# Kernel optimization log

Hardware: AMD Instinct MI355X
Metric: run time of the kernel (lower is better)

The kernel has to match this reference:

```python
import jax, jax.numpy as jnp
import numpy as np

B, K, BIN = 16, 2048, 256
GRU, EMB, HID = 1024, 1024, 1024
H, KV = 16, 4
D = HID // H          # 64 head dim
NREP = H // KV        # 4 GQA repeat factor


def rotate_half(x):
    x1, x2 = jnp.split(x, 2, axis=-1)
    return jnp.concatenate((-x2, x1), axis=-1)


def setup_inputs() -> dict:
    key = jax.random.key(0)
    ks = jax.random.split(key, 8)
    h = jax.random.normal(ks[0], (B, K, GRU), dtype=jnp.float32)
    # real RoPE frequency tables, shape (BIN, D)
    inv_freq = 1.0 / (10000.0 ** (jnp.arange(0, D, 2, dtype=jnp.float32) / D))
    t = jnp.arange(BIN, dtype=jnp.float32)
    freqs = jnp.outer(t, inv_freq)                      # (BIN, D/2)
    emb = jnp.concatenate((freqs, freqs), axis=-1)      # (BIN, D)
    freqs_cos, freqs_sin = jnp.cos(emb), jnp.sin(emb)
    s = lambda fan: 1.0 / np.sqrt(fan).astype(np.float32)
    Wq = jax.random.normal(ks[1], (H * D, EMB), jnp.float32) * s(EMB)
    Wk = jax.random.normal(ks[2], (KV * D, GRU), jnp.float32) * s(GRU)
    Wv = jax.random.normal(ks[3], (KV * D, GRU), jnp.float32) * s(GRU)
    Wo = jax.random.normal(ks[4], (EMB, H * D), jnp.float32) * s(H * D)
    output_queries = jax.random.normal(ks[5], (BIN, EMB), jnp.float32)
    Wr = jax.random.normal(ks[6], (2, EMB), jnp.float32) * s(EMB)
    br = jnp.zeros((2,), jnp.float32)
    return {"h": h, "freqs_cos": freqs_cos, "freqs_sin": freqs_sin,
            "Wq": Wq, "Wk": Wk, "Wv": Wv, "Wo": Wo,
            "output_queries": output_queries, "Wr": Wr, "br": br}


def reference(h, freqs_cos, freqs_sin, Wq, Wk, Wv, Wo, output_queries, Wr, br):
    # KV projections from GRU history: (B, K, KV, D)
    k = (h @ Wk.T).reshape(B, K, KV, D)
    v = (h @ Wv.T).reshape(B, K, KV, D)
    # Queries are batch-invariant learned tokens: (BIN, H, D)
    q = (output_queries @ Wq.T).reshape(BIN, H, D)
    cos = freqs_cos[:, None, :]  # (BIN, 1, D) broadcast over heads
    sin = freqs_sin[:, None, :]
    q = q * cos + rotate_half(q) * sin
    # GQA: repeat_interleave KV heads to H heads
    k_rep = jnp.repeat(k, NREP, axis=2)  # (B, K, H, D)
    v_rep = jnp.repeat(v, NREP, axis=2)
    scores = jnp.einsum('qhd,bkhd->bhqk', q, k_rep) / np.sqrt(D).astype(np.float32)
    attn = jax.nn.softmax(scores, axis=-1)               # dropout p=0 (eval)
    out = jnp.einsum('bhqk,bkhd->bqhd', attn, v_rep).reshape(B, BIN, H * D)
    z = out @ Wo.T                                        # (B, BIN, EMB)
    return z @ Wr.T + br                                  # (B, BIN, 2)
```

## Files before the change

### kernel.cpp

```cpp
#include <hip/hip_runtime.h>

typedef __attribute__((ext_vector_type(8))) short short8;
typedef __attribute__((ext_vector_type(4))) float f32x4;
typedef __attribute__((ext_vector_type(16))) float f32x16;

#define DEV static __device__ __forceinline__

DEV unsigned short f2bf(float f) {
  unsigned int u = __float_as_uint(f);
  u += 0x7fff + ((u >> 16) & 1);
  return (unsigned short)(u >> 16);
}

DEV unsigned int cvtpk(float lo, float hi) {
  unsigned int r;
  asm("v_cvt_pk_bf16_f32 %0, %1, %2" : "=v"(r) : "v"(lo), "v"(hi));
  return r;
}

DEV float max3f(float a, float b, float c) {
  float r;
  asm("v_max3_f32 %0, %1, %2, %3" : "=v"(r) : "v"(a), "v"(b), "v"(c));
  return r;
}

DEV f32x4 mfma16(short8 a, short8 b, f32x4 c) {
  return __builtin_amdgcn_mfma_f32_16x16x32_bf16(a, b, c, 0, 0, 0);
}

DEV f32x16 mfma32(short8 a, short8 b, f32x16 c) {
  return __builtin_amdgcn_mfma_f32_32x32x16_bf16(a, b, c, 0, 0, 0);
}

DEV void gl_lds16(const void* g, void* l) {
  __builtin_amdgcn_global_load_lds((const __attribute__((address_space(1))) void*)g,
                                   (__attribute__((address_space(3))) void*)l, 16, 0, 0);
}

__global__ __launch_bounds__(256) void cvtB_kernel(const float* __restrict__ Wq,
                                                   const float* __restrict__ Wk,
                                                   const float* __restrict__ Wv,
                                                   unsigned short* __restrict__ wqb,
                                                   unsigned short* __restrict__ wkvb) {
  int id = blockIdx.x * 256 + threadIdx.x;
  int e = id * 4;
  float4 v;
  unsigned short* d;
  if (e < 1048576)      { v = *(const float4*)(Wq + e);             d = wqb + e; }
  else if (e < 1310720) { v = *(const float4*)(Wk + (e - 1048576)); d = wkvb + (e - 1048576); }
  else                  { v = *(const float4*)(Wv + (e - 1310720)); d = wkvb + 262144 + (e - 1310720); }
  uint2 pk;
  pk.x = cvtpk(v.x, v.y);
  pk.y = cvtpk(v.z, v.w);
  *(uint2*)d = pk;
}

__global__ __launch_bounds__(256) void wrp_partial(const float* __restrict__ Wr,
                                                   const float* __restrict__ Wo,
                                                   float* __restrict__ part) {
  int blk = blockIdx.x;
  int tid = threadIdx.x;
  float a0[4] = {0.f,0.f,0.f,0.f};
  float a1[4] = {0.f,0.f,0.f,0.f};
  int e0 = blk * 64;
  for (int e = e0; e < e0 + 64; e++) {
    float w0 = Wr[e];
    float w1 = Wr[1024 + e];
    #pragma unroll
    for (int j4 = 0; j4 < 4; j4++) {
      float wo = Wo[(size_t)e * 1024 + j4 * 256 + tid];
      a0[j4] += w0 * wo;
      a1[j4] += w1 * wo;
    }
  }
  #pragma unroll
  for (int j4 = 0; j4 < 4; j4++) {
    part[blk * 2048 + 0    + j4 * 256 + tid] = a0[j4];
    part[blk * 2048 + 1024 + j4 * 256 + tid] = a1[j4];
  }
}

__global__ __launch_bounds__(256) void wrp_reduce(const float* __restrict__ part,
                                                  float* __restrict__ Wrp) {
  int id = blockIdx.x * 256 + threadIdx.x;
  float s = 0.f;
  #pragma unroll
  for (int blk = 0; blk < 16; blk++) s += part[blk * 2048 + id];
  Wrp[id] = s;
}

__global__ __launch_bounds__(512, 2) void gemm_kv(const float* __restrict__ A,
                                                  const unsigned short* __restrict__ Bb,
                                                  unsigned short* __restrict__ ok,
                                                  unsigned short* __restrict__ vrm) {
  __shared__ unsigned short Asl[3][4096];
  __shared__ unsigned short Bsl[3][16384];

  int bid = blockIdx.x;
  int sw = (bid & 7) * 32 + (bid >> 3);
  int m0 = sw * 128;

  int tid = threadIdx.x;
  int w = tid >> 6, l = tid & 63;
  int l4 = l >> 4, l15 = l & 15;

  int arow = tid >> 2, ac = tid & 3;
  const float* ga = A + (size_t)(m0 + arow) * 1024 + ac * 8;
  int awb = arow * 64 + ((ac ^ ((arow >> 1) & 3)) * 16);

  const unsigned short* gbB = Bb + (size_t)(tid >> 2) * 1024
                                 + (((tid & 3) ^ ((tid >> 3) & 3)) * 8);

  int fsw = (l4 ^ ((l15 >> 1) & 3)) * 16;
  int aoff = l15 * 64 + fsw;
  int boff = (w * 64 + l15) * 64 + fsw;

  f32x4 acc[8][4];
  #pragma unroll
  for (int i = 0; i < 8; i++)
    #pragma unroll
    for (int j = 0; j < 4; j++) acc[i][j] = (f32x4)(0.f);

  float4 aXx, aXy, aYx, aYy;

  #define LOADA(T, RX, RY)                                                  \
    { const float* gA = ga + (T) * 32;                                      \
      RX = *(const float4*)(gA);                                            \
      RY = *(const float4*)(gA + 4); }

  #define STAGEB(SB, T)                                                     \
    { const unsigned short* b0p = gbB + (T) * 32;                           \
      gl_lds16(b0p,          (char*)Bsl[SB] + tid * 16);                    \
      gl_lds16(b0p + 131072, (char*)Bsl[SB] + 8192  + tid * 16);            \
      gl_lds16(b0p + 262144, (char*)Bsl[SB] + 16384 + tid * 16);            \
      gl_lds16(b0p + 393216, (char*)Bsl[SB] + 24576 + tid * 16); }

  #define WRITEA(WB, RX, RY)                                                \
    { union { short8 s; unsigned int u[4]; } af;                            \
      af.u[0] = cvtpk(RX.x, RX.y); af.u[1] = cvtpk(RX.z, RX.w);             \
      af.u[2] = cvtpk(RY.x, RY.y); af.u[3] = cvtpk(RY.z, RY.w);             \
      *(short8*)((char*)Asl[WB] + awb) = af.s; }

  #define COMPUTE(CB)                                                       \
    { const char* Ab = (const char*)Asl[CB];                                \
      const char* Bf = (const char*)Bsl[CB];                                \
      short8 bfr[4];                                                        \
      _Pragma("unroll")                                                     \
      for (int j = 0; j < 4; j++)                                           \
        bfr[j] = *(const short8*)(Bf + boff + j * 1024);                    \
      __builtin_amdgcn_s_setprio(1);                                        \
      _Pragma("unroll")                                                     \
      for (int i = 0; i < 8; i++) {                                         \
        short8 af = *(const short8*)(Ab + aoff + i * 1024);                 \
        _Pragma("unroll")                                                   \
        for (int j = 0; j < 4; j++)                                         \
          acc[i][j] = mfma16(af, bfr[j], acc[i][j]);                        \
      }                                                                     \
      __builtin_amdgcn_s_setprio(0); }

  #define ENDSTEP                                                           \
    { asm volatile("s_waitcnt vmcnt(6)" ::: "memory");                      \
      asm volatile("s_waitcnt lgkmcnt(0)" ::: "memory");                    \
      __builtin_amdgcn_s_barrier();                                         \
      __builtin_amdgcn_sched_barrier(0); }

  LOADA(0, aXx, aXy);
  STAGEB(0, 0);
  WRITEA(0, aXx, aXy);
  LOADA(1, aXx, aXy);
  STAGEB(1, 1);
  asm volatile("s_waitcnt vmcnt(6)" ::: "memory");
  asm volatile("s_waitcnt lgkmcnt(0)" ::: "memory");
  __builtin_amdgcn_s_barrier();
  __builtin_amdgcn_sched_barrier(0);

  #define STEPE(T, CB, WB, SB)                                              \
    { LOADA((T) + 2, aYx, aYy); STAGEB(SB, (T) + 2);                        \
      COMPUTE(CB); WRITEA(WB, aXx, aXy); ENDSTEP }
  #define STEPO(T, CB, WB, SB)                                              \
    { LOADA((T) + 2, aXx, aXy); STAGEB(SB, (T) + 2);                        \
      COMPUTE(CB); WRITEA(WB, aYx, aYy); ENDSTEP }

  #pragma unroll 1
  for (int tb = 0; tb < 30; tb += 6) {
    STEPE(tb + 0, 0, 1, 2);
    STEPO(tb + 1, 1, 2, 0);
    STEPE(tb + 2, 2, 0, 1);
    STEPO(tb + 3, 0, 1, 2);
    STEPE(tb + 4, 1, 2, 0);
    STEPO(tb + 5, 2, 0, 1);
  }
  COMPUTE(0);
  WRITEA(1, aXx, aXy);
  asm volatile("s_waitcnt vmcnt(0)" ::: "memory");
  asm volatile("s_waitcnt lgkmcnt(0)" ::: "memory");
  __builtin_amdgcn_s_barrier();
  __builtin_amdgcn_sched_barrier(0);
  COMPUTE(1);

  #undef LOADA
  #undef STAGEB
  #undef WRITEA
  #undef COMPUTE
  #undef ENDSTEP
  #undef STEPE
  #undef STEPO

  #pragma unroll
  for (int i = 0; i < 8; i++)
    #pragma unroll
    for (int j = 0; j < 4; j++) {
      int n = w * 64 + j * 16 + l15;
      int kvv = n >> 6, d = n & 63;
      #pragma unroll
      for (int r = 0; r < 4; r++) {
        int m = m0 + i * 16 + l4 * 4 + r;
        int bb = m >> 11, kk = m & 2047;
        unsigned short val = f2bf(acc[i][j][r]);
        if (kvv < 4)
          ok[((size_t)(bb * 4 + kvv) * 2048 + kk) * 64 + d] = val;
        else
          vrm[((size_t)(bb * 4 + (kvv - 4)) * 2048 + kk) * 64 + d] = val;
      }
    }
}

__global__ __launch_bounds__(256) void vtr_kernel(const unsigned short* __restrict__ vrm,
                                                  unsigned short* __restrict__ vt) {
  __shared__ unsigned short T[64][72];
  int g = blockIdx.x >> 5;
  int kt = blockIdx.x & 31;
  int tid = threadIdx.x;
  int r = tid >> 2, c0 = (tid & 3) * 16;

  const unsigned short* src = vrm + ((size_t)g * 2048 + kt * 64) * 64;
  *(short8*)&T[r][c0]     = *(const short8*)(src + (size_t)r * 64 + c0);
  *(short8*)&T[r][c0 + 8] = *(const short8*)(src + (size_t)r * 64 + c0 + 8);
  __syncthreads();

  int d = tid >> 2;
  unsigned short* dst = vt + (size_t)g * 131072 + (size_t)d * 2048 + kt * 64 + (tid & 3) * 16;
  short8 o0, o1;
  #pragma unroll
  for (int j = 0; j < 8; j++) {
    o0[j] = (short)T[(tid & 3) * 16 + j][d];
    o1[j] = (short)T[(tid & 3) * 16 + 8 + j][d];
  }
  *(short8*)dst = o0;
  *(short8*)(dst + 8) = o1;
}

__global__ __launch_bounds__(256) void gemm_q(const float* __restrict__ A,
                                              const unsigned short* __restrict__ Bb,
                                              float* __restrict__ of) {
  __shared__ unsigned short Asm[2][4096];
  __shared__ unsigned short Bsm[2][4096];

  int bid = blockIdx.x;
  int ksplit = bid >> 4;
  int m0 = ((bid >> 3) & 1) * 128;
  int n0 = (bid & 7) * 128;
  int t0 = ksplit * 8;
  constexpr int nt = 8;

  int tid = threadIdx.x;
  int w = tid >> 6, l = tid & 63;
  int l4 = l >> 4, l15 = l & 15;
  int wm = w >> 1, wn = w & 1;

  int ra = w * 32 + (l >> 1);
  int rx = (l >> 2) & 3;
  const float* ga = A + (size_t)(m0 + ra) * 1024 + t0 * 32 + (l & 1) * 16;
  int pw0 = (2 * (l & 1) + 0) ^ rx;
  int pw1 = (2 * (l & 1) + 1) ^ rx;
  int awb0 = ra * 64 + pw0 * 16;
  int awb1 = ra * 64 + pw1 * 16;

  int rb = w * 32 + (l >> 2);
  int cb = ((l & 3) ^ ((l >> 3) & 3)) * 8;
  const unsigned short* gb = Bb + (size_t)(n0 + rb) * 1024 + t0 * 32 + cb;

  int qsw = l4 ^ ((l15 >> 1) & 3);
  int arb = (wm * 64 + l15) * 64 + qsw * 16;
  int brb = (wn * 64 + l15) * 64 + qsw * 16;

  f32x4 acc[4][4];
  #pragma unroll
  for (int i = 0; i < 4; i++)
    #pragma unroll
    for (int j = 0; j < 4; j++) acc[i][j] = (f32x4)(0.f);

  float4 fa0, fa1, fa2, fa3;

  #define LOADA(tt)                                                        \
    { const float* gA = ga + (tt) * 32;                                    \
      fa0 = *(const float4*)(gA);                                          \
      fa1 = *(const float4*)(gA + 4);                                      \
      fa2 = *(const float4*)(gA + 8);                                      \
      fa3 = *(const float4*)(gA + 12); }

  #define WRITEA(bufi)                                                     \
    { union { short8 s; unsigned int u[4]; } t0u, t1u;                     \
      t0u.u[0] = cvtpk(fa0.x, fa0.y); t0u.u[1] = cvtpk(fa0.z, fa0.w);      \
      t0u.u[2] = cvtpk(fa1.x, fa1.y); t0u.u[3] = cvtpk(fa1.z, fa1.w);      \
      t1u.u[0] = cvtpk(fa2.x, fa2.y); t1u.u[1] = cvtpk(fa2.z, fa2.w);      \
      t1u.u[2] = cvtpk(fa3.x, fa3.y); t1u.u[3] = cvtpk(fa3.z, fa3.w);      \
      *(short8*)((char*)Asm[bufi] + awb0) = t0u.s;                         \
      *(short8*)((char*)Asm[bufi] + awb1) = t1u.s; }

  #define STAGEB(bufi, tt)                                                 \
    { char* lb = (char*)Bsm[bufi] + w * 2048;                              \
      const unsigned short* gB = gb + (tt) * 32;                           \
      gl_lds16(gB, lb);                                                    \
      gl_lds16(gB + 16384, lb + 1024); }

  LOADA(0);
  STAGEB(0, 0);
  WRITEA(0);
  __syncthreads();

  for (int t = 0; t < nt; t++) {
    int buf = t & 1;
    if (t + 1 < nt) {
      LOADA(t + 1);
      STAGEB(buf ^ 1, t + 1);
    }
    short8 af[4], bfg[4];
    #pragma unroll
    for (int i = 0; i < 4; i++)
      af[i] = *(const short8*)((char*)Asm[buf] + arb + i * 1024);
    #pragma unroll
    for (int j = 0; j < 4; j++)
      bfg[j] = *(const short8*)((char*)Bsm[buf] + brb + j * 1024);
    #pragma unroll
    for (int i = 0; i < 4; i++)
      #pragma unroll
      for (int j = 0; j < 4; j++)
        acc[i][j] = mfma16(af[i], bfg[j], acc[i][j]);
    if (t + 1 < nt) WRITEA(buf ^ 1);
    __syncthreads();
  }
  #undef LOADA
  #undef WRITEA
  #undef STAGEB

  float* o = of + (size_t)ksplit * 262144;
  #pragma unroll
  for (int i = 0; i < 4; i++)
    #pragma unroll
    for (int j = 0; j < 4; j++) {
      int n = n0 + wn * 64 + j * 16 + l15;
      #pragma unroll
      for (int r = 0; r < 4; r++) {
        int m = m0 + wm * 64 + i * 16 + l4 * 4 + r;
        o[(size_t)m * 1024 + n] = acc[i][j][r];
      }
    }
}

__global__ __launch_bounds__(256) void rope_kernel(const float* __restrict__ qp,
                                                   const float* __restrict__ cosb,
                                                   const float* __restrict__ sinb,
                                                   unsigned short* __restrict__ qb) {
  int id = blockIdx.x * 256 + threadIdx.x;
  int qrow = id >> 10, hd = id & 1023, hh = hd >> 6, d = hd & 63;
  int od = hh * 64 + ((d < 32) ? d + 32 : d - 32);
  float v = 0.f, o = 0.f;
  #pragma unroll
  for (int s4 = 0; s4 < 4; s4++) {
    v += qp[s4 * 262144 + qrow * 1024 + hd];
    o += qp[s4 * 262144 + qrow * 1024 + od];
  }
  if (d < 32) o = -o;
  float c = cosb[qrow * 64 + d];
  float s = sinb[qrow * 64 + d];
  float outv = (v * c + o * s) * 0.18033688011112042f;
  qb[((size_t)hh * 256 + qrow) * 64 + d] = f2bf(outv);
}

__global__ __launch_bounds__(256) void attn_kernel(const unsigned short* __restrict__ qb,
                                                   const unsigned short* __restrict__ kb,
                                                   const unsigned short* __restrict__ vb,
                                                   const float* __restrict__ Wrp,
                                                   float* __restrict__ part) {
  __shared__ unsigned short Kt[3][4096];
  __shared__ unsigned short Vt[3][4096];

  int bid = blockIdx.x;
  int x = bid & 7, mid = (bid >> 3) & 7, top2 = bid >> 6;
  int g = mid * 8 + x;
  int b = g >> 2, kvh = g & 3;
  int split = top2 >> 3;
  int top = top2 & 7;
  int hl = top >> 1, qh = top & 1;
  int h = kvh * 4 + hl;

  int tid = threadIdx.x;
  int w = tid >> 6, l = tid & 63;
  int q31 = l & 31, L = l >> 5;
  int qg = qh * 128 + w * 32 + q31;

  const unsigned short* kg = kb + (size_t)(b * 4 + kvh) * 2048 * 64;
  const unsigned short* vg = vb + (size_t)(b * 4 + kvh) * 64 * 2048;

  short8 qf[4];
  #pragma unroll
  for (int c = 0; c < 4; c++)
    qf[c] = *(const short8*)&qb[((size_t)h * 256 + qg) * 64 + c * 16 + L * 8];

  f32x16 Ot[2];
  Ot[0] = (f32x16)(0.f); Ot[1] = (f32x16)(0.f);
  float m = -1e30f, lsum = 0.f;

  int ksrow = tid >> 3, kslot = tid & 7;
  const unsigned short* ksrc = kg + (size_t)ksrow * 64 + ((kslot ^ (ksrow & 7)) * 8);
  int vsrow = tid >> 2, vslot = tid & 3;
  const unsigned short* vsrc = vg + (size_t)vsrow * 2048 + ((vslot ^ ((vsrow >> 1) & 3)) * 8);

  int tb0 = split * 16;

  #define STAGE(bufi, tt)                                                       \
    { gl_lds16(ksrc + (size_t)((tt) * 2 + 0) * 2048, (char*)Kt[bufi] + tid * 16);        \
      gl_lds16(ksrc + (size_t)((tt) * 2 + 1) * 2048, (char*)Kt[bufi] + 4096 + tid * 16); \
      gl_lds16(vsrc + ((tt) * 2 + 0) * 32,           (char*)Vt[bufi] + tid * 16);        \
      gl_lds16(vsrc + ((tt) * 2 + 1) * 32,           (char*)Vt[bufi] + 4096 + tid * 16); }

  #define COMPUTE(CB)                                                           \
    _Pragma("unroll")                                                           \
    for (int sub = 0; sub < 2; sub++) {                                         \
      const char* Kb = (const char*)Kt[CB] + sub * 4096;                        \
      const char* Vb = (const char*)Vt[CB] + sub * 4096;                        \
      f32x16 st = (f32x16)(0.f);                                                \
      _Pragma("unroll")                                                         \
      for (int c = 0; c < 4; c++) {                                             \
        int row = q31;                                                          \
        int byt = row * 128 + (((c * 2 + L) ^ (row & 7)) * 16);                 \
        short8 kf = *(const short8*)(Kb + byt);                                 \
        st = mfma32(kf, qf[c], st);                                             \
      }                                                                         \
      float g0 = max3f(st[0], st[1], st[2]);                                    \
      float g1 = max3f(st[3], st[4], st[5]);                                    \
      float g2 = max3f(st[6], st[7], st[8]);                                    \
      float g3 = max3f(st[9], st[10], st[11]);                                  \
      float g4 = max3f(st[12], st[13], st[14]);                                 \
      float mx = fmaxf(max3f(g0, g1, g2), max3f(g3, g4, st[15]));               \
      mx = fmaxf(mx, __shfl_xor(mx, 32));                                       \
      if (!__all(mx <= m + 8.f)) {                                              \
        float mnew = fmaxf(m, mx);                                              \
        float corr = exp2f(m - mnew);                                           \
        lsum *= corr;                                                           \
        _Pragma("unroll")                                                       \
        for (int db = 0; db < 2; db++)                                          \
          _Pragma("unroll")                                                     \
          for (int r = 0; r < 16; r++) Ot[db][r] *= corr;                       \
        m = mnew;                                                               \
      }                                                                         \
      float p[16];                                                              \
      float ls = 0.f;                                                           \
      _Pragma("unroll")                                                         \
      for (int r = 0; r < 16; r++) {                                            \
        p[r] = exp2f(st[r] - m);                                                \
        ls += p[r];                                                             \
      }                                                                         \
      lsum += ls;                                                               \
      unsigned int pw[2][4];                                                    \
      _Pragma("unroll")                                                         \
      for (int kc = 0; kc < 2; kc++) {                                          \
        unsigned int A0 = cvtpk(p[kc * 8 + 0], p[kc * 8 + 1]);                  \
        unsigned int A1 = cvtpk(p[kc * 8 + 2], p[kc * 8 + 3]);                  \
        unsigned int B0 = cvtpk(p[kc * 8 + 4], p[kc * 8 + 5]);                  \
        unsigned int B1 = cvtpk(p[kc * 8 + 6], p[kc * 8 + 7]);                  \
        asm volatile("v_permlane32_swap_b32 %0, %1" : "+v"(A0), "+v"(B0));      \
        asm volatile("v_permlane32_swap_b32 %0, %1" : "+v"(A1), "+v"(B1));      \
        pw[kc][0] = A0; pw[kc][1] = A1; pw[kc][2] = B0; pw[kc][3] = B1;         \
      }                                                                         \
      _Pragma("unroll")                                                         \
      for (int db = 0; db < 2; db++) {                                          \
        int drow = db * 32 + q31;                                               \
        _Pragma("unroll")                                                       \
        for (int kc = 0; kc < 2; kc++) {                                        \
          int byt = drow * 64 + (((kc * 2 + L) ^ ((drow >> 1) & 3)) * 16);      \
          short8 vf = *(const short8*)(Vb + byt);                               \
          short8 pf;                                                            \
          {                                                                     \
            union { short8 s; unsigned int u[4]; } uu;                          \
            uu.u[0] = pw[kc][0]; uu.u[1] = pw[kc][1];                           \
            uu.u[2] = pw[kc][2]; uu.u[3] = pw[kc][3];                           \
            pf = uu.s;                                                          \
          }                                                                     \
          Ot[db] = mfma32(vf, pf, Ot[db]);                                      \
        }                                                                       \
      }                                                                         \
    }

  #define E8                                                                    \
    { asm volatile("s_waitcnt vmcnt(8)" ::: "memory");                          \
      __builtin_amdgcn_s_barrier();                                             \
      __builtin_amdgcn_sched_barrier(0); }

  STAGE(0, tb0 + 0);
  STAGE(1, tb0 + 1);
  asm volatile("s_waitcnt vmcnt(8)" ::: "memory");
  __builtin_amdgcn_s_barrier();
  __builtin_amdgcn_sched_barrier(0);

  #pragma unroll 1
  for (int tb = 0; tb < 12; tb += 3) {
    STAGE(2, tb0 + tb + 2); COMPUTE(0) E8;
    STAGE(0, tb0 + tb + 3); COMPUTE(1) E8;
    STAGE(1, tb0 + tb + 4); COMPUTE(2) E8;
  }
  STAGE(2, tb0 + 14); COMPUTE(0) E8;
  STAGE(0, tb0 + 15); COMPUTE(1) E8;
  COMPUTE(2)
  asm volatile("s_waitcnt vmcnt(0)" ::: "memory");
  __builtin_amdgcn_s_barrier();
  __builtin_amdgcn_sched_barrier(0);
  COMPUTE(0)

  #undef STAGE
  #undef COMPUTE
  #undef E8

  lsum += __shfl_xor(lsum, 32);

  float a0 = 0.f, a1 = 0.f;
  #pragma unroll
  for (int db = 0; db < 2; db++)
    #pragma unroll
    for (int rq = 0; rq < 4; rq++) {
      int dbase = db * 32 + rq * 8 + L * 4;
      float4 w0v = *(const float4*)(Wrp + h * 64 + dbase);
      float4 w1v = *(const float4*)(Wrp + 1024 + h * 64 + dbase);
      #pragma unroll
      for (int j = 0; j < 4; j++) {
        float o = Ot[db][rq * 4 + j];
        a0 += o * ((const float*)&w0v)[j];
        a1 += o * ((const float*)&w1v)[j];
      }
    }
  a0 += __shfl_xor(a0, 32);
  a1 += __shfl_xor(a1, 32);

  if (L == 0) {
    size_t base = ((((size_t)(b * 16 + h) * 256 + qg) * 2) + split) * 4;
    float4 r4;
    r4.x = m; r4.y = lsum; r4.z = a0; r4.w = a1;
    *(float4*)&part[base] = r4;
  }
}

__global__ __launch_bounds__(256) void final_kernel(const float* __restrict__ part,
                                                    const float* __restrict__ br,
                                                    float* __restrict__ out) {
  int id = blockIdx.x * 256 + threadIdx.x;
  int c = id & 1, q = (id >> 1) & 255, b = id >> 9;
  float s = br[c];
  #pragma unroll
  for (int hh = 0; hh < 16; hh++) {
    size_t base = (((size_t)(b * 16 + hh) * 256 + q) * 2) * 4;
    float4 f0 = *(const float4*)&part[base];
    float4 f1 = *(const float4*)&part[base + 4];
    float mm = fmaxf(f0.x, f1.x);
    float w0 = exp2f(f0.x - mm), w1 = exp2f(f1.x - mm);
    float den = w0 * f0.y + w1 * f1.y;
    float num = (c == 0) ? (w0 * f0.z + w1 * f1.z) : (w0 * f0.w + w1 * f1.w);
    s += num / den;
  }
  out[id] = s;
}

extern "C" void kernel_launch(void* const* d_in, const int* in_sizes, int n_in,
                              void* d_out, int out_size, void* d_ws, size_t ws_size,
                              hipStream_t stream) {
  const float* h    = (const float*)d_in[0];
  const float* fcos = (const float*)d_in[1];
  const float* fsin = (const float*)d_in[2];
  const float* Wq   = (const float*)d_in[3];
  const float* Wk   = (const float*)d_in[4];
  const float* Wv   = (const float*)d_in[5];
  const float* Wo   = (const float*)d_in[6];
  const float* oq   = (const float*)d_in[7];
  const float* Wr   = (const float*)d_in[8];
  const float* br   = (const float*)d_in[9];
  float* out = (float*)d_out;

  char* ws = (char*)d_ws;
  unsigned short* kbuf = (unsigned short*)(ws);
  unsigned short* vbuf = (unsigned short*)(ws + 16777216);
  float* qpart         = (float*)(ws + 33554432);
  unsigned short* qbf  = (unsigned short*)(ws + 37748736);
  float* wpart         = (float*)(ws + 38273024);
  float* Wrp           = (float*)(ws + 38404096);
  float* apart         = (float*)(ws + 38412288);
  unsigned short* wqb  = (unsigned short*)(ws + 42606592);
  unsigned short* wkvb = (unsigned short*)(ws + 44703744);
  unsigned short* vrm  = (unsigned short*)(ws + 45752320);

  cvtB_kernel<<<dim3(1536), dim3(256), 0, stream>>>(Wq, Wk, Wv, wqb, wkvb);
  wrp_partial<<<dim3(16), dim3(256), 0, stream>>>(Wr, Wo, wpart);
  wrp_reduce<<<dim3(8), dim3(256), 0, stream>>>(wpart, Wrp);
  gemm_q<<<dim3(64), dim3(256), 0, stream>>>(oq, wqb, qpart);
  rope_kernel<<<dim3(1024), dim3(256), 0, stream>>>(qpart, fcos, fsin, qbf);
  gemm_kv<<<dim3(256), dim3(512), 0, stream>>>(h, wkvb, kbuf, vrm);
  vtr_kernel<<<dim3(2048), dim3(256), 0, stream>>>(vrm, vbuf);
  attn_kernel<<<dim3(1024), dim3(256), 0, stream>>>(qbf, kbuf, vbuf, Wrp, apart);
  final_kernel<<<dim3(32), dim3(256), 0, stream>>>(apart, br, out);
}
```

Measured before the change: 147.6 us.

## Replace triple-buffered gemm_kv pipeline with a simpler double-buffered loop

The KV projection GEMM moves from a three-stage LDS ring with two-deep prefetch and vmcnt(6) partial waits to a two-buffer ping-pong loop that prefetches one tile ahead and waits for all loads (vmcnt(0)) each step. This cuts LDS per block by a third and drops one set of A staging registers, which could raise occupancy. In exchange it reduces how far global loads can run ahead of compute, so memory latency is more exposed, and the loop is no longer hand-unrolled.

```diff
diff --git a/kernel.cpp b/kernel.cpp
--- a/kernel.cpp
+++ b/kernel.cpp
@@ -93,8 +93,8 @@
                                                   const unsigned short* __restrict__ Bb,
                                                   unsigned short* __restrict__ ok,
                                                   unsigned short* __restrict__ vrm) {
-  __shared__ unsigned short Asl[3][4096];
-  __shared__ unsigned short Bsl[3][16384];
+  __shared__ unsigned short Asl[2][4096];
+  __shared__ unsigned short Bsl[2][16384];
 
   int bid = blockIdx.x;
   int sw = (bid & 7) * 32 + (bid >> 3);
@@ -121,12 +121,12 @@
     #pragma unroll
     for (int j = 0; j < 4; j++) acc[i][j] = (f32x4)(0.f);
 
-  float4 aXx, aXy, aYx, aYy;
-
-  #define LOADA(T, RX, RY)                                                  \
+  float4 aX, aY;
+
+  #define LOADA(T)                                                          \
     { const float* gA = ga + (T) * 32;                                      \
-      RX = *(const float4*)(gA);                                            \
-      RY = *(const float4*)(gA + 4); }
+      aX = *(const float4*)(gA);                                            \
+      aY = *(const float4*)(gA + 4); }
 
   #define STAGEB(SB, T)                                                     \
     { const unsigned short* b0p = gbB + (T) * 32;                           \
@@ -135,10 +135,10 @@
       gl_lds16(b0p + 262144, (char*)Bsl[SB] + 16384 + tid * 16);            \
       gl_lds16(b0p + 393216, (char*)Bsl[SB] + 24576 + tid * 16); }
 
-  #define WRITEA(WB, RX, RY)                                                \
+  #define WRITEA(WB)                                                        \
     { union { short8 s; unsigned int u[4]; } af;                            \
-      af.u[0] = cvtpk(RX.x, RX.y); af.u[1] = cvtpk(RX.z, RX.w);             \
-      af.u[2] = cvtpk(RY.x, RY.y); af.u[3] = cvtpk(RY.z, RY.w);             \
+      af.u[0] = cvtpk(aX.x, aX.y); af.u[1] = cvtpk(aX.z, aX.w);             \
+      af.u[2] = cvtpk(aY.x, aY.y); af.u[3] = cvtpk(aY.z, aY.w);             \
       *(short8*)((char*)Asl[WB] + awb) = af.s; }
 
   #define COMPUTE(CB)                                                       \
@@ -158,53 +158,33 @@
       }                                                                     \
       __builtin_amdgcn_s_setprio(0); }
 
-  #define ENDSTEP                                                           \
-    { asm volatile("s_waitcnt vmcnt(6)" ::: "memory");                      \
-      asm volatile("s_waitcnt lgkmcnt(0)" ::: "memory");                    \
-      __builtin_amdgcn_s_barrier();                                         \
-      __builtin_amdgcn_sched_barrier(0); }
-
-  LOADA(0, aXx, aXy);
+  LOADA(0);
   STAGEB(0, 0);
-  WRITEA(0, aXx, aXy);
-  LOADA(1, aXx, aXy);
-  STAGEB(1, 1);
-  asm volatile("s_waitcnt vmcnt(6)" ::: "memory");
-  asm volatile("s_waitcnt lgkmcnt(0)" ::: "memory");
-  __builtin_amdgcn_s_barrier();
-  __builtin_amdgcn_sched_barrier(0);
-
-  #define STEPE(T, CB, WB, SB)                                              \
-    { LOADA((T) + 2, aYx, aYy); STAGEB(SB, (T) + 2);                        \
-      COMPUTE(CB); WRITEA(WB, aXx, aXy); ENDSTEP }
-  #define STEPO(T, CB, WB, SB)                                              \
-    { LOADA((T) + 2, aXx, aXy); STAGEB(SB, (T) + 2);                        \
-      COMPUTE(CB); WRITEA(WB, aYx, aYy); ENDSTEP }
-
-  #pragma unroll 1
-  for (int tb = 0; tb < 30; tb += 6) {
-    STEPE(tb + 0, 0, 1, 2);
-    STEPO(tb + 1, 1, 2, 0);
-    STEPE(tb + 2, 2, 0, 1);
-    STEPO(tb + 3, 0, 1, 2);
-    STEPE(tb + 4, 1, 2, 0);
-    STEPO(tb + 5, 2, 0, 1);
-  }
-  COMPUTE(0);
-  WRITEA(1, aXx, aXy);
+  WRITEA(0);
   asm volatile("s_waitcnt vmcnt(0)" ::: "memory");
   asm volatile("s_waitcnt lgkmcnt(0)" ::: "memory");
   __builtin_amdgcn_s_barrier();
   __builtin_amdgcn_sched_barrier(0);
-  COMPUTE(1);
+
+  #pragma unroll 1
+  for (int t = 0; t < 32; t++) {
+    int buf = t & 1;
+    if (t + 1 < 32) {
+      LOADA(t + 1);
+      STAGEB(buf ^ 1, t + 1);
+    }
+    COMPUTE(buf);
+    if (t + 1 < 32) WRITEA(buf ^ 1);
+    asm volatile("s_waitcnt vmcnt(0)" ::: "memory");
+    asm volatile("s_waitcnt lgkmcnt(0)" ::: "memory");
+    __builtin_amdgcn_s_barrier();
+    __builtin_amdgcn_sched_barrier(0);
+  }
 
   #undef LOADA
   #undef STAGEB
   #undef WRITEA
   #undef COMPUTE
-  #undef ENDSTEP
-  #undef STEPE
-  #undef STEPO
 
   #pragma unroll
   for (int i = 0; i < 8; i++)
```

Measured after the change: 160.5 us. 1.09x slower.
